# Optimization experiments

Measured on AMD Instinct MI355X. Metric: run time of the kernel, lower is better.

Reference implementation:

```python
import jax, jax.numpy as jnp
import numpy as np

B, T, C, H = 16, 4096, 256, 256

def setup_inputs() -> dict:
    key = jax.random.key(0)
    kx, kwi, kbi, kwh, kbh = jax.random.split(key, 5)
    s = 1.0 / np.sqrt(C)
    return {
        "x": jax.random.normal(kx, (B, T, C), dtype=jnp.float32),
        "Wi": jax.random.uniform(kwi, (H, C), dtype=jnp.float32, minval=-s, maxval=s),
        "bi": jax.random.uniform(kbi, (H,), dtype=jnp.float32, minval=-s, maxval=s),
        "Wh": jax.random.uniform(kwh, (H, H), dtype=jnp.float32, minval=-s, maxval=s),
        "bh": jax.random.uniform(kbh, (H,), dtype=jnp.float32, minval=-s, maxval=s),
    }

def reference(x, Wi, bi, Wh, bh):
    # Faithful to the source: Cell computes tanh(i2h(x) + h2h(x)) -- both
    # linears applied to x_t, the hidden state is never consumed, so there
    # is no recurrence and all timesteps can be computed in one fused pass.
    # hidden_states: [B, T, H]
    hidden_states = jnp.tanh(
        jnp.einsum("btc,hc->bth", x, Wi) + bi
        + jnp.einsum("btc,hc->bth", x, Wh) + bh
    )
    h_last = hidden_states[:, -1, :]  # h after the loop
    return (hidden_states, h_last)
```

## Files before the change

kernel.cpp:

```cpp
#include <hip/hip_runtime.h>


using short8 = __attribute__((ext_vector_type(8))) short;
using f32x4  = __attribute__((ext_vector_type(4))) float;

constexpr int Bn = 16, Tn = 4096, Cn = 256, Hn = 256;
constexpr int Mn    = Bn * Tn;
constexpr int BM    = 32;
constexpr int NBLK  = 256;
constexpr int TILES = Mn / BM;
constexpr int ITERS = TILES / NBLK;

__device__ inline unsigned pack2_bf16(float a, float b) {
  unsigned ua = __float_as_uint(a);
  unsigned ub = __float_as_uint(b);
  ua += 0x7fffu + ((ua >> 16) & 1u);
  ub += 0x7fffu + ((ub >> 16) & 1u);
  return (ua >> 16) | (ub & 0xffff0000u);
}

__global__ __launch_bounds__(256) void prep_kernel(
    const float* __restrict__ Wi, const float* __restrict__ bi,
    const float* __restrict__ Wh, const float* __restrict__ bh,
    unsigned short* __restrict__ Wc, float* __restrict__ bc) {
  int idx = blockIdx.x * 256 + threadIdx.x;
  float w = Wi[idx] + Wh[idx];
  unsigned u = __float_as_uint(w);
  u += 0x7fffu + ((u >> 16) & 1u);
  Wc[idx] = (unsigned short)(u >> 16);
  if (blockIdx.x == 0) bc[threadIdx.x] = bi[threadIdx.x] + bh[threadIdx.x];
}

__global__ __launch_bounds__(1024, 4) void gemm_tanh_kernel(
    const float* __restrict__ x, const unsigned short* __restrict__ Wc,
    const float* __restrict__ bc, float* __restrict__ out) {
  __shared__ __align__(16) unsigned short Asm[2][BM * Cn];

  const int tid  = threadIdx.x;
  const int lane = tid & 63;
  const int wave = tid >> 6;
  const int rid  = lane & 15;
  const int kgrp = lane >> 4;
  const int col  = wave * 16 + rid;

  short8 bf[8];
#pragma unroll
  for (int ks = 0; ks < 8; ks++)
    bf[ks] = *(const short8*)&Wc[col * Cn + ks * 32 + kgrp * 8];
  const float bias = bc[col];

  const int sr  = tid >> 5;
  const int sc  = tid & 31;
  const int swz = ((sc ^ (sr & 7)) << 3);

  f32x4 acc[2];
  acc[0] = (f32x4)0.f;
  acc[1] = (f32x4)0.f;

  float4 v0, v1;

  {
    const float4* src =
        (const float4*)(x + (size_t)(blockIdx.x * BM + sr) * Cn + sc * 8);
    v0 = src[0];
    v1 = src[1];
    uint4 p;
    p.x = pack2_bf16(v0.x, v0.y);
    p.y = pack2_bf16(v0.z, v0.w);
    p.z = pack2_bf16(v1.x, v1.y);
    p.w = pack2_bf16(v1.z, v1.w);
    *(uint4*)&Asm[0][sr * Cn + swz] = p;
  }
  __syncthreads();

  for (int t = 0; t < ITERS; t++) {
    const int cur = t & 1;
    const int m0  = (blockIdx.x + t * NBLK) * BM;

    if (t + 1 < ITERS) {
      const float4* src =
          (const float4*)(x + (size_t)(m0 + NBLK * BM + sr) * Cn + sc * 8);
      v0 = src[0];
      v1 = src[1];
    }

#pragma unroll
    for (int ks = 0; ks < 8; ks++) {
#pragma unroll
      for (int mt = 0; mt < 2; mt++) {
        int row = mt * 16 + rid;
        short8 a = *(const short8*)
            &Asm[cur][row * Cn + ((((ks << 2) | kgrp) ^ (rid & 7)) << 3)];
        acc[mt] = __builtin_amdgcn_mfma_f32_16x16x32_bf16(a, bf[ks], acc[mt],
                                                          0, 0, 0);
      }
    }

    if (t + 1 < ITERS) {
      uint4 p;
      p.x = pack2_bf16(v0.x, v0.y);
      p.y = pack2_bf16(v0.z, v0.w);
      p.z = pack2_bf16(v1.x, v1.y);
      p.w = pack2_bf16(v1.z, v1.w);
      *(uint4*)&Asm[cur ^ 1][sr * Cn + swz] = p;
    }

#pragma unroll
    for (int mt = 0; mt < 2; mt++) {
#pragma unroll
      for (int r = 0; r < 4; r++) {
        int m   = m0 + mt * 16 + kgrp * 4 + r;
        float v = acc[mt][r] + bias;
        float tv = 1.f - 2.f / (__expf(2.f * v) + 1.f);
        out[(size_t)m * Hn + col] = tv;
        if ((m & (Tn - 1)) == (Tn - 1))
          out[(size_t)Mn * Hn + (size_t)(m >> 12) * Hn + col] = tv;
      }
      acc[mt] = (f32x4)0.f;
    }

    if (t + 1 < ITERS) __syncthreads();
  }
}

extern "C" void kernel_launch(void* const* d_in, const int* in_sizes, int n_in,
                              void* d_out, int out_size, void* d_ws,
                              size_t ws_size, hipStream_t stream) {
  (void)in_sizes; (void)n_in; (void)out_size; (void)ws_size;
  const float* x  = (const float*)d_in[0];
  const float* Wi = (const float*)d_in[1];
  const float* bi = (const float*)d_in[2];
  const float* Wh = (const float*)d_in[3];
  const float* bh = (const float*)d_in[4];
  float* out = (float*)d_out;

  unsigned short* Wc = (unsigned short*)d_ws;
  float* bc = (float*)((char*)d_ws + (size_t)Hn * Cn * sizeof(unsigned short));

  prep_kernel<<<(Hn * Cn) / 256, 256, 0, stream>>>(Wi, bi, Wh, bh, Wc, bc);
  gemm_tanh_kernel<<<NBLK, 1024, 0, stream>>>(x, Wc, bc, out);
}
```

Measured before the change: 133.3 us.

## Replace persistent double-buffered loop with one 32-row tile per block

The kernel no longer runs 256 persistent blocks that loop over tiles with a double-buffered LDS prefetch. It now launches one block per 32-row tile (2048 blocks) with a single LDS buffer, issuing the global x load before the weight fragment loads, and raises the launch-bounds occupancy hint. Load/compute overlap now comes from the hardware interleaving many resident blocks instead of explicit software pipelining. In exchange, every block reloads the combined weight fragments and bias, which adds redundant L2 traffic and per-block setup cost.

```diff
diff --git a/kernel.cpp b/kernel.cpp
--- a/kernel.cpp
+++ b/kernel.cpp
@@ -5,11 +5,9 @@
 using f32x4  = __attribute__((ext_vector_type(4))) float;
 
 constexpr int Bn = 16, Tn = 4096, Cn = 256, Hn = 256;
-constexpr int Mn    = Bn * Tn;
-constexpr int BM    = 32;
-constexpr int NBLK  = 256;
-constexpr int TILES = Mn / BM;
-constexpr int ITERS = TILES / NBLK;
+constexpr int Mn = Bn * Tn;
+constexpr int BM = 32;
+constexpr int NBLK = Mn / BM;
 
 __device__ inline unsigned pack2_bf16(float a, float b) {
   unsigned ua = __float_as_uint(a);
@@ -31,10 +29,10 @@
   if (blockIdx.x == 0) bc[threadIdx.x] = bi[threadIdx.x] + bh[threadIdx.x];
 }
 
-__global__ __launch_bounds__(1024, 4) void gemm_tanh_kernel(
+__global__ __launch_bounds__(1024, 8) void gemm_tanh_kernel(
     const float* __restrict__ x, const unsigned short* __restrict__ Wc,
     const float* __restrict__ bc, float* __restrict__ out) {
-  __shared__ __align__(16) unsigned short Asm[2][BM * Cn];
+  __shared__ __align__(16) unsigned short Asm[BM * Cn];
 
   const int tid  = threadIdx.x;
   const int lane = tid & 63;
@@ -42,6 +40,14 @@
   const int rid  = lane & 15;
   const int kgrp = lane >> 4;
   const int col  = wave * 16 + rid;
+  const int m0   = blockIdx.x * BM;
+
+  const int sr = tid >> 5;
+  const int sc = tid & 31;
+  const float4* src =
+      (const float4*)(x + (size_t)(m0 + sr) * Cn + sc * 8);
+  float4 v0 = src[0];
+  float4 v1 = src[1];
 
   short8 bf[8];
 #pragma unroll
@@ -49,77 +55,42 @@
     bf[ks] = *(const short8*)&Wc[col * Cn + ks * 32 + kgrp * 8];
   const float bias = bc[col];
 
-  const int sr  = tid >> 5;
-  const int sc  = tid & 31;
-  const int swz = ((sc ^ (sr & 7)) << 3);
-
-  f32x4 acc[2];
-  acc[0] = (f32x4)0.f;
-  acc[1] = (f32x4)0.f;
-
-  float4 v0, v1;
-
   {
-    const float4* src =
-        (const float4*)(x + (size_t)(blockIdx.x * BM + sr) * Cn + sc * 8);
-    v0 = src[0];
-    v1 = src[1];
     uint4 p;
     p.x = pack2_bf16(v0.x, v0.y);
     p.y = pack2_bf16(v0.z, v0.w);
     p.z = pack2_bf16(v1.x, v1.y);
     p.w = pack2_bf16(v1.z, v1.w);
-    *(uint4*)&Asm[0][sr * Cn + swz] = p;
+    *(uint4*)&Asm[sr * Cn + ((sc ^ (sr & 7)) << 3)] = p;
   }
   __syncthreads();
 
-  for (int t = 0; t < ITERS; t++) {
-    const int cur = t & 1;
-    const int m0  = (blockIdx.x + t * NBLK) * BM;
-
-    if (t + 1 < ITERS) {
-      const float4* src =
-          (const float4*)(x + (size_t)(m0 + NBLK * BM + sr) * Cn + sc * 8);
-      v0 = src[0];
-      v1 = src[1];
+  f32x4 acc[2];
+  acc[0] = (f32x4)0.f;
+  acc[1] = (f32x4)0.f;
+#pragma unroll
+  for (int ks = 0; ks < 8; ks++) {
+#pragma unroll
+    for (int mt = 0; mt < 2; mt++) {
+      int row = mt * 16 + rid;
+      short8 a = *(const short8*)
+          &Asm[row * Cn + ((((ks << 2) | kgrp) ^ (rid & 7)) << 3)];
+      acc[mt] = __builtin_amdgcn_mfma_f32_16x16x32_bf16(a, bf[ks], acc[mt],
+                                                        0, 0, 0);
     }
+  }
 
 #pragma unroll
-    for (int ks = 0; ks < 8; ks++) {
+  for (int mt = 0; mt < 2; mt++) {
 #pragma unroll
-      for (int mt = 0; mt < 2; mt++) {
-        int row = mt * 16 + rid;
-        short8 a = *(const short8*)
-            &Asm[cur][row * Cn + ((((ks << 2) | kgrp) ^ (rid & 7)) << 3)];
-        acc[mt] = __builtin_amdgcn_mfma_f32_16x16x32_bf16(a, bf[ks], acc[mt],
-                                                          0, 0, 0);
-      }
+    for (int r = 0; r < 4; r++) {
+      int m   = m0 + mt * 16 + kgrp * 4 + r;
+      float v = acc[mt][r] + bias;
+      float tv = 1.f - 2.f / (__expf(2.f * v) + 1.f);
+      out[(size_t)m * Hn + col] = tv;
+      if ((m & (Tn - 1)) == (Tn - 1))
+        out[(size_t)Mn * Hn + (size_t)(m >> 12) * Hn + col] = tv;
     }
-
-    if (t + 1 < ITERS) {
-      uint4 p;
-      p.x = pack2_bf16(v0.x, v0.y);
-      p.y = pack2_bf16(v0.z, v0.w);
-      p.z = pack2_bf16(v1.x, v1.y);
-      p.w = pack2_bf16(v1.z, v1.w);
-      *(uint4*)&Asm[cur ^ 1][sr * Cn + swz] = p;
-    }
-
-#pragma unroll
-    for (int mt = 0; mt < 2; mt++) {
-#pragma unroll
-      for (int r = 0; r < 4; r++) {
-        int m   = m0 + mt * 16 + kgrp * 4 + r;
-        float v = acc[mt][r] + bias;
-        float tv = 1.f - 2.f / (__expf(2.f * v) + 1.f);
-        out[(size_t)m * Hn + col] = tv;
-        if ((m & (Tn - 1)) == (Tn - 1))
-          out[(size_t)Mn * Hn + (size_t)(m >> 12) * Hn + col] = tv;
-      }
-      acc[mt] = (f32x4)0.f;
-    }
-
-    if (t + 1 < ITERS) __syncthreads();
   }
 }
 
```

Result: slower. 142.0 us (+6.5%).
